# Kernel tuning notes

Hardware: AMD Instinct MI355X
Metric: run time of the kernel (lower is better)

## Reference

```python
import jax, jax.numpy as jnp
import numpy as np

N_NODES = 50000
N_EDGES = 800000
IN_CH = 64
HID = 64
EDGE_DIM = 16


def _glorot(key, shape):
    fan_in, fan_out = shape[0], shape[1]
    lim = (6.0 / (fan_in + fan_out)) ** 0.5
    return jax.random.uniform(key, shape, jnp.float32, -lim, lim)


def setup_inputs() -> dict:
    key = jax.random.key(0)
    ks = jax.random.split(key, 12)
    x = jax.random.normal(ks[0], (N_NODES, IN_CH), jnp.float32)
    edge_index = jax.random.randint(ks[1], (2, N_EDGES), 0, N_NODES, jnp.int64)
    edge_attr = jax.random.normal(ks[2], (N_EDGES, EDGE_DIM), jnp.float32)
    # SAGEConv1: lin_l (aggregated neighbors, with bias) + lin_r (root, no bias)
    W1l = _glorot(ks[3], (IN_CH, HID)); b1l = jnp.zeros((HID,), jnp.float32)
    W1r = _glorot(ks[4], (IN_CH, HID))
    # SAGEConv2
    W2l = _glorot(ks[5], (HID, HID)); b2l = jnp.zeros((HID,), jnp.float32)
    W2r = _glorot(ks[6], (HID, HID))
    # edge MLP: Linear(2*HID+EDGE_DIM -> HID), ReLU, Linear(HID -> 1)
    Wm1 = _glorot(ks[7], (2 * HID + EDGE_DIM, HID))
    bm1 = jnp.zeros((HID,), jnp.float32)
    Wm2 = _glorot(ks[8], (HID, 1))
    bm2 = jnp.zeros((1,), jnp.float32)
    return dict(x=x, edge_index=edge_index, edge_attr=edge_attr,
                W1l=W1l, b1l=b1l, W1r=W1r,
                W2l=W2l, b2l=b2l, W2r=W2r,
                Wm1=Wm1, bm1=bm1, Wm2=Wm2, bm2=bm2)


def _sage_conv(x, src, dst, deg_inv, Wl, bl, Wr):
    # mean aggregation of source-node features at destination nodes
    n = x.shape[0]
    agg = jax.ops.segment_sum(x[src], dst, num_segments=n)  # [N, d]
    agg = agg * deg_inv  # mean over incoming edges
    return agg @ Wl + bl + x @ Wr


def reference(x, edge_index, edge_attr, W1l, b1l, W1r, W2l, b2l, W2r, Wm1, bm1, Wm2, bm2):
    src, dst = edge_index[0], edge_index[1]
    n = x.shape[0]
    # in-degree (over dst), clamped to 1 as in PyG mean aggregation
    deg = jax.ops.segment_sum(jnp.ones((src.shape[0],), x.dtype), dst, num_segments=n)
    deg_inv = (1.0 / jnp.maximum(deg, 1.0))[:, None]  # [N,1]

    h = jax.nn.relu(_sage_conv(x, src, dst, deg_inv, W1l, b1l, W1r))
    h = jax.nn.relu(_sage_conv(h, src, dst, deg_inv, W2l, b2l, W2r))

    # gather endpoint embeddings + concat with edge features -> MLP score
    edge_input = jnp.concatenate([h[src], h[dst], edge_attr], axis=-1)  # [E, 2H+De]
    hidden = jax.nn.relu(edge_input @ Wm1 + bm1)
    return (hidden @ Wm2 + bm2).squeeze(-1)  # [E]
```

## Files before the change

kernel.cpp:

```cpp
#include <hip/hip_runtime.h>
#include <hip/hip_bf16.h>


#define C 64
#define KP 168
#define SK 136
#define TILE_E 64

typedef short short8 __attribute__((ext_vector_type(8)));
typedef float f32x4 __attribute__((ext_vector_type(4)));

__device__ __forceinline__ unsigned short f2bf(float f) {
    unsigned int u = __float_as_uint(f);
    return (unsigned short)((u + 0x7FFFu + ((u >> 16) & 1u)) >> 16);
}
__device__ __forceinline__ unsigned int pack2(float lo, float hi) {
    return (unsigned int)f2bf(lo) | ((unsigned int)f2bf(hi) << 16);
}
__device__ __forceinline__ float bflo(unsigned int u) { return __uint_as_float(u << 16); }
__device__ __forceinline__ float bfhi(unsigned int u) { return __uint_as_float(u & 0xFFFF0000u); }

__global__ void deg_count_ea(const int* __restrict__ dst, int* __restrict__ degi,
                             const float* __restrict__ ea, unsigned short* __restrict__ eaB,
                             int E, int doEa) {
    int i = blockIdx.x * blockDim.x + threadIdx.x;
    if (i < E) atomicAdd(&degi[dst[i]], 1);
    if (doEa && i < 2 * E) {
        const float4* p = (const float4*)(ea + (size_t)i * 8);
        float4 a = p[0], b = p[1];
        uint4 o;
        o.x = pack2(a.x, a.y); o.y = pack2(a.z, a.w);
        o.z = pack2(b.x, b.y); o.w = pack2(b.z, b.w);
        *(uint4*)(eaB + (size_t)i * 8) = o;
    }
}

__global__ __launch_bounds__(256) void scan_partial(const int* __restrict__ degi,
        int* __restrict__ rowptr, int* __restrict__ partials, int N) {
    __shared__ int sWs[4];
    int t = threadIdx.x, b = blockIdx.x;
    int g0 = b * 1024 + t * 4;
    int v0 = (g0 + 0 < N) ? degi[g0 + 0] : 0;
    int v1 = (g0 + 1 < N) ? degi[g0 + 1] : 0;
    int v2 = (g0 + 2 < N) ? degi[g0 + 2] : 0;
    int v3 = (g0 + 3 < N) ? degi[g0 + 3] : 0;
    int tsum = v0 + v1 + v2 + v3;
    int lane = t & 63, w = t >> 6;
    int incl = tsum;
    #pragma unroll
    for (int m = 1; m < 64; m <<= 1) {
        int y = __shfl_up(incl, m, 64);
        if (lane >= m) incl += y;
    }
    if (lane == 63) sWs[w] = incl;
    __syncthreads();
    int wprefix = 0;
    for (int i = 0; i < w; ++i) wprefix += sWs[i];
    int run = wprefix + incl - tsum;
    if (g0 + 0 < N) rowptr[g0 + 0] = run; run += v0;
    if (g0 + 1 < N) rowptr[g0 + 1] = run; run += v1;
    if (g0 + 2 < N) rowptr[g0 + 2] = run; run += v2;
    if (g0 + 3 < N) rowptr[g0 + 3] = run;
    if (t == 255) partials[b] = wprefix + incl;
}

__global__ void scan_offsets(const int* __restrict__ partials, int* __restrict__ offsets, int nb) {
    int lane = threadIdx.x;
    int v = (lane < nb) ? partials[lane] : 0;
    int incl = v;
    #pragma unroll
    for (int m = 1; m < 64; m <<= 1) {
        int y = __shfl_up(incl, m, 64);
        if (lane >= m) incl += y;
    }
    if (lane < nb) offsets[lane] = incl - v;
}

__global__ void scan_add(int* __restrict__ rowptr, const int* __restrict__ offsets,
                         int* __restrict__ cursor, const int* __restrict__ degi,
                         float* __restrict__ deg_inv, int N, int E) {
    int i = blockIdx.x * blockDim.x + threadIdx.x;
    if (i < N) {
        int r = rowptr[i] + offsets[i >> 10];
        rowptr[i] = r;
        cursor[i] = r;
        deg_inv[i] = 1.0f / fmaxf((float)degi[i], 1.0f);
    }
    if (i == 0) rowptr[N] = E;
}

__global__ void fill_csr(const int* __restrict__ src, const int* __restrict__ dst,
                         int* __restrict__ cursor, int* __restrict__ eSrc, int E) {
    int e = blockIdx.x * blockDim.x + threadIdx.x;
    if (e < E) {
        int p = atomicAdd(&cursor[dst[e]], 1);
        eSrc[p] = src[e];
    }
}

__global__ void to_bf16(const float* __restrict__ in, unsigned short* __restrict__ outb, int n8) {
    int i = blockIdx.x * blockDim.x + threadIdx.x;
    if (i >= n8) return;
    const float4* p = (const float4*)(in + (size_t)i * 8);
    float4 a = p[0], b = p[1];
    uint4 o;
    o.x = pack2(a.x, a.y); o.y = pack2(a.z, a.w);
    o.z = pack2(b.x, b.y); o.w = pack2(b.z, b.w);
    *(uint4*)(outb + (size_t)i * 8) = o;
}

__global__ __launch_bounds__(256) void csr_agg_bf16(const unsigned short* __restrict__ fB,
        const int* __restrict__ rowptr, const int* __restrict__ eSrc,
        const float* __restrict__ deg_inv, unsigned short* __restrict__ aggB, int N) {
    int node = blockIdx.x * 4 + (threadIdx.x >> 6);
    if (node >= N) return;
    int lane = threadIdx.x & 63;
    int s8 = lane >> 3, ci = lane & 7;
    int row = rowptr[node], end = rowptr[node + 1];
    float a[8] = {0.f, 0.f, 0.f, 0.f, 0.f, 0.f, 0.f, 0.f};
    int j = row;
    for (; j + 16 <= end; j += 16) {
        int sA = eSrc[j + s8];
        int sB = eSrc[j + 8 + s8];
        uint4 vA = *(const uint4*)(fB + (size_t)sA * C + ci * 8);
        uint4 vB = *(const uint4*)(fB + (size_t)sB * C + ci * 8);
        a[0] += bflo(vA.x); a[1] += bfhi(vA.x);
        a[2] += bflo(vA.y); a[3] += bfhi(vA.y);
        a[4] += bflo(vA.z); a[5] += bfhi(vA.z);
        a[6] += bflo(vA.w); a[7] += bfhi(vA.w);
        a[0] += bflo(vB.x); a[1] += bfhi(vB.x);
        a[2] += bflo(vB.y); a[3] += bfhi(vB.y);
        a[4] += bflo(vB.z); a[5] += bfhi(vB.z);
        a[6] += bflo(vB.w); a[7] += bfhi(vB.w);
    }
    for (; j < end; j += 8) {
        if (j + s8 < end) {
            int s = eSrc[j + s8];
            uint4 v = *(const uint4*)(fB + (size_t)s * C + ci * 8);
            a[0] += bflo(v.x); a[1] += bfhi(v.x);
            a[2] += bflo(v.y); a[3] += bfhi(v.y);
            a[4] += bflo(v.z); a[5] += bfhi(v.z);
            a[6] += bflo(v.w); a[7] += bfhi(v.w);
        }
    }
    #pragma unroll
    for (int m = 8; m < 64; m <<= 1)
        #pragma unroll
        for (int k = 0; k < 8; ++k)
            a[k] += __shfl_xor(a[k], m, 64);
    if (s8 == 0) {
        float di = deg_inv[node];
        uint4 o;
        o.x = pack2(a[0] * di, a[1] * di);
        o.y = pack2(a[2] * di, a[3] * di);
        o.z = pack2(a[4] * di, a[5] * di);
        o.w = pack2(a[6] * di, a[7] * di);
        *(uint4*)(aggB + (size_t)node * C + ci * 8) = o;
    }
}

__global__ __launch_bounds__(256) void dense_mfma(
        const unsigned short* __restrict__ aB, const unsigned short* __restrict__ xB,
        const float* __restrict__ Wl, const float* __restrict__ Wr,
        const float* __restrict__ bl, unsigned short* __restrict__ hOut, int N) {
    __shared__ unsigned short sW[C * SK];
    __shared__ unsigned short sAB[C * SK];
    int t = threadIdx.x;
    int lane = t & 63, w = t >> 6;
    int l15 = lane & 15, quad = lane >> 4;
    int n0 = blockIdx.x * 64;

    for (int i = t; i < 128 * C; i += 256) {
        int k = i >> 6, n = i & 63;
        float v = (k < C) ? Wl[k * C + n] : Wr[(k - C) * C + n];
        sW[n * SK + k] = f2bf(v);
    }
    for (int i = t; i < 64 * 16; i += 256) {
        int r = i >> 4, ch = i & 15;
        int node = n0 + r;
        uint4 v = {0u, 0u, 0u, 0u};
        if (node < N)
            v = (ch < 8) ? *(const uint4*)(aB + (size_t)node * C + ch * 8)
                         : *(const uint4*)(xB + (size_t)node * C + (ch - 8) * 8);
        *(uint4*)&sAB[r * SK + ch * 8] = v;
    }
    __syncthreads();

    short8 bW[4][4];
    #pragma unroll
    for (int t4 = 0; t4 < 4; ++t4)
        #pragma unroll
        for (int kc = 0; kc < 4; ++kc)
            bW[t4][kc] = *(const short8*)&sW[(t4 * 16 + l15) * SK + kc * 32 + quad * 8];
    float blr[4];
    #pragma unroll
    for (int t4 = 0; t4 < 4; ++t4) blr[t4] = bl[t4 * 16 + l15];

    f32x4 acc[4] = {{0.f, 0.f, 0.f, 0.f}, {0.f, 0.f, 0.f, 0.f},
                    {0.f, 0.f, 0.f, 0.f}, {0.f, 0.f, 0.f, 0.f}};
    #pragma unroll
    for (int kc = 0; kc < 4; ++kc) {
        short8 a = *(const short8*)&sAB[(w * 16 + l15) * SK + kc * 32 + quad * 8];
        #pragma unroll
        for (int t4 = 0; t4 < 4; ++t4)
            acc[t4] = __builtin_amdgcn_mfma_f32_16x16x32_bf16(a, bW[t4][kc], acc[t4], 0, 0, 0);
    }
    __syncthreads();

    #pragma unroll
    for (int t4 = 0; t4 < 4; ++t4)
        #pragma unroll
        for (int r = 0; r < 4; ++r) {
            int rl = w * 16 + quad * 4 + r;
            sW[rl * 72 + t4 * 16 + l15] = f2bf(fmaxf(acc[t4][r] + blr[t4], 0.f));
        }
    __syncthreads();
    for (int i = t; i < 64 * 8; i += 256) {
        int r = i >> 3, c8 = i & 7;
        int node = n0 + r;
        if (node < N)
            *(uint4*)(hOut + (size_t)node * C + c8 * 8) = *(const uint4*)&sW[r * 72 + c8 * 8];
    }
}

template <bool EAB>
__device__ __forceinline__ void gather_rows(const unsigned short* __restrict__ hB,
        const unsigned short* __restrict__ eaB, const float* __restrict__ ea,
        int s, int d, int idxc, int quad,
        uint4& u0, uint4& u1, uint4& u2, uint4& u3, uint4& u4) {
    const uint4* ps = (const uint4*)(hB + (size_t)s * C);
    const uint4* pd = (const uint4*)(hB + (size_t)d * C);
    u0 = ps[quad];
    u1 = ps[4 + quad];
    u2 = pd[quad];
    u3 = pd[4 + quad];
    u4.x = 0u; u4.y = 0u; u4.z = 0u; u4.w = 0u;
    if (quad < 2) {
        if (EAB) {
            u4 = *(const uint4*)(eaB + (size_t)idxc * 16 + quad * 8);
        } else {
            const float4* pe = (const float4*)(ea + (size_t)idxc * 16 + quad * 8);
            float4 f0 = pe[0], f1 = pe[1];
            u4.x = pack2(f0.x, f0.y); u4.y = pack2(f0.z, f0.w);
            u4.z = pack2(f1.x, f1.y); u4.w = pack2(f1.z, f1.w);
        }
    }
}

template <bool EAB>
__global__ __launch_bounds__(256) void edge_mlp_pipe(
        const unsigned short* __restrict__ hB, const int* __restrict__ src,
        const int* __restrict__ dst, const float* __restrict__ ea,
        const unsigned short* __restrict__ eaB,
        const float* __restrict__ Wm1, const float* __restrict__ bm1,
        const float* __restrict__ Wm2, const float* __restrict__ bm2,
        float* __restrict__ out, int E, int nTiles) {
    __shared__ unsigned short sW[C * KP];
    int t = threadIdx.x;
    int lane = t & 63, w = t >> 6;
    int l15 = lane & 15, quad = lane >> 4;

    for (int i = t; i < C * 3; i += 256) {
        int r = i / 3, cc = 144 + (i % 3) * 8;
        uint4 z = {0u, 0u, 0u, 0u};
        *(uint4*)&sW[r * KP + cc] = z;
    }
    for (int i = t; i < 144 * C; i += 256) {
        int k = i >> 6, n = i & 63;
        sW[n * KP + k] = f2bf(Wm1[i]);
    }
    __syncthreads();

    short8 bW[4][5];
    #pragma unroll
    for (int t4 = 0; t4 < 4; ++t4)
        #pragma unroll
        for (int kc = 0; kc < 5; ++kc)
            bW[t4][kc] = *(const short8*)&sW[(t4 * 16 + l15) * KP + kc * 32 + quad * 8];
    float bmr[4], w2r[4];
    #pragma unroll
    for (int t4 = 0; t4 < 4; ++t4) {
        int j = t4 * 16 + l15;
        bmr[t4] = bm1[j];
        w2r[t4] = Wm2[j];
    }
    float bb = bm2[0];

    int stride = gridDim.x;
    int lbase = w * 16 + l15;

    int tile = blockIdx.x;
    int idxc = min(tile * TILE_E + lbase, E - 1);
    int s = src[idxc], d = dst[idxc];
    int tileN = tile + stride;
    int idxNc = (tileN < nTiles) ? min(tileN * TILE_E + lbase, E - 1) : idxc;
    int sN = src[idxNc], dN = dst[idxNc];
    uint4 cu0, cu1, cu2, cu3, cu4;
    gather_rows<EAB>(hB, eaB, ea, s, d, idxc, quad, cu0, cu1, cu2, cu3, cu4);

    while (true) {
        bool hasNext = (tileN < nTiles);
        uint4 nu0, nu1, nu2, nu3, nu4;
        gather_rows<EAB>(hB, eaB, ea, sN, dN, idxNc, quad, nu0, nu1, nu2, nu3, nu4);
        int tileNN = tileN + stride;
        int idxNNc = (tileNN < nTiles) ? min(tileNN * TILE_E + lbase, E - 1) : idxNc;
        int sNN = src[idxNNc], dNN = dst[idxNNc];

        short8 a0 = *(short8*)&cu0, a1 = *(short8*)&cu1, a2 = *(short8*)&cu2,
               a3 = *(short8*)&cu3, a4 = *(short8*)&cu4;
        f32x4 acc[4] = {{0.f, 0.f, 0.f, 0.f}, {0.f, 0.f, 0.f, 0.f},
                        {0.f, 0.f, 0.f, 0.f}, {0.f, 0.f, 0.f, 0.f}};
        #pragma unroll
        for (int t4 = 0; t4 < 4; ++t4) {
            acc[t4] = __builtin_amdgcn_mfma_f32_16x16x32_bf16(a0, bW[t4][0], acc[t4], 0, 0, 0);
            acc[t4] = __builtin_amdgcn_mfma_f32_16x16x32_bf16(a1, bW[t4][1], acc[t4], 0, 0, 0);
            acc[t4] = __builtin_amdgcn_mfma_f32_16x16x32_bf16(a2, bW[t4][2], acc[t4], 0, 0, 0);
            acc[t4] = __builtin_amdgcn_mfma_f32_16x16x32_bf16(a3, bW[t4][3], acc[t4], 0, 0, 0);
            acc[t4] = __builtin_amdgcn_mfma_f32_16x16x32_bf16(a4, bW[t4][4], acc[t4], 0, 0, 0);
        }

        float sres[4];
        #pragma unroll
        for (int r = 0; r < 4; ++r) {
            float v = 0.f;
            #pragma unroll
            for (int t4 = 0; t4 < 4; ++t4)
                v += fmaxf(acc[t4][r] + bmr[t4], 0.f) * w2r[t4];
            #pragma unroll
            for (int m = 1; m < 16; m <<= 1)
                v += __shfl_xor(v, m, 16);
            sres[r] = v;
        }
        if (l15 == 0) {
            int e0 = tile * TILE_E;
            #pragma unroll
            for (int r = 0; r < 4; ++r) {
                int e = e0 + w * 16 + quad * 4 + r;
                if (e < E) out[e] = sres[r] + bb;
            }
        }

        if (!hasNext) break;
        tile = tileN; tileN = tileNN;
        idxc = idxNc; idxNc = idxNNc;
        s = sN; sN = sNN; d = dN; dN = dNN;
        cu0 = nu0; cu1 = nu1; cu2 = nu2; cu3 = nu3; cu4 = nu4;
    }
}

extern "C" void kernel_launch(void* const* d_in, const int* in_sizes, int n_in,
                              void* d_out, int out_size, void* d_ws, size_t ws_size,
                              hipStream_t stream) {
    const float* x   = (const float*)d_in[0];
    const int*   ei  = (const int*)d_in[1];
    const float* ea  = (const float*)d_in[2];
    const float* W1l = (const float*)d_in[3];
    const float* b1l = (const float*)d_in[4];
    const float* W1r = (const float*)d_in[5];
    const float* W2l = (const float*)d_in[6];
    const float* b2l = (const float*)d_in[7];
    const float* W2r = (const float*)d_in[8];
    const float* Wm1 = (const float*)d_in[9];
    const float* bm1 = (const float*)d_in[10];
    const float* Wm2 = (const float*)d_in[11];
    const float* bm2 = (const float*)d_in[12];
    float* out = (float*)d_out;

    const int N = in_sizes[0] / C;
    const int E = in_sizes[1] / 2;
    const int* src = ei;
    const int* dst = ei + E;

    char* wsb = (char*)d_ws;
    int npad = (N + 1023) & ~1023;
    float* deg_inv = (float*)wsb;                wsb += (size_t)npad * 4;
    unsigned short* xB   = (unsigned short*)wsb; wsb += (size_t)npad * C * 2;
    unsigned short* h1B  = (unsigned short*)wsb; wsb += (size_t)npad * C * 2;
    unsigned short* h2B  = (unsigned short*)wsb; wsb += (size_t)npad * C * 2;
    unsigned short* aggB = (unsigned short*)wsb; wsb += (size_t)npad * C * 2;
    int* degi    = (int*)wsb;                    wsb += (size_t)npad * 4;
    int* rowptr  = (int*)wsb;                    wsb += (size_t)(npad + 64) * 4;
    int* cursor  = (int*)wsb;                    wsb += (size_t)npad * 4;
    int* eSrc    = (int*)wsb;                    wsb += (size_t)E * 4;
    int* partials = (int*)wsb;                   wsb += 64 * 4;
    int* offsets  = (int*)wsb;                   wsb += 64 * 4;
    unsigned short* eaB = (unsigned short*)wsb;
    size_t used = (size_t)(wsb - (char*)d_ws);
    int useEaB = (ws_size >= used + (size_t)E * 16 * 2) ? 1 : 0;

    int tpb = 256;
    int nb = (N + 1023) / 1024;

    hipMemsetAsync(degi, 0, (size_t)N * sizeof(int), stream);
    deg_count_ea<<<(2 * E + tpb - 1) / tpb, tpb, 0, stream>>>(dst, degi, ea, eaB, E, useEaB);
    to_bf16<<<((N * C / 8) + tpb - 1) / tpb, tpb, 0, stream>>>(x, xB, N * C / 8);
    scan_partial<<<nb, tpb, 0, stream>>>(degi, rowptr, partials, N);
    scan_offsets<<<1, 64, 0, stream>>>(partials, offsets, nb);
    scan_add<<<(N + tpb - 1) / tpb, tpb, 0, stream>>>(rowptr, offsets, cursor, degi, deg_inv, N, E);
    fill_csr<<<(E + tpb - 1) / tpb, tpb, 0, stream>>>(src, dst, cursor, eSrc, E);

    csr_agg_bf16<<<(N + 3) / 4, tpb, 0, stream>>>(xB, rowptr, eSrc, deg_inv, aggB, N);
    dense_mfma<<<(N + 63) / 64, tpb, 0, stream>>>(aggB, xB, W1l, W1r, b1l, h1B, N);

    csr_agg_bf16<<<(N + 3) / 4, tpb, 0, stream>>>(h1B, rowptr, eSrc, deg_inv, aggB, N);
    dense_mfma<<<(N + 63) / 64, tpb, 0, stream>>>(aggB, h1B, W2l, W2r, b2l, h2B, N);

    int nTiles = (E + TILE_E - 1) / TILE_E;
    int grid = nTiles < 2048 ? nTiles : 2048;
    if (useEaB)
        edge_mlp_pipe<true><<<grid, tpb, 0, stream>>>(h2B, src, dst, ea, eaB,
                Wm1, bm1, Wm2, bm2, out, E, nTiles);
    else
        edge_mlp_pipe<false><<<grid, tpb, 0, stream>>>(h2B, src, dst, ea, eaB,
                Wm1, bm1, Wm2, bm2, out, E, nTiles);
}
```

Baseline: 314.9 us.

## Fuse CSR aggregation into dense MFMA layer and merge small prep/scan kernels

Each SAGE layer's neighbor mean aggregation now runs inside the dense MFMA kernel. Each wave aggregates 16 nodes straight into shared memory, so the aggB global round-trip and one launch per layer go away. The x-to-bf16 conversion is folded into the degree/edge-attr prep kernel, and the offsets scan is merged into scan_add. The cost is that the fused kernel runs only 782 blocks with serial per-node aggregation per wave, so it has less parallelism for hiding gather latency than the earlier 12.5k-block aggregation kernel.

```diff
diff --git a/kernel.cpp b/kernel.cpp
--- a/kernel.cpp
+++ b/kernel.cpp
@@ -20,9 +20,10 @@
 __device__ __forceinline__ float bflo(unsigned int u) { return __uint_as_float(u << 16); }
 __device__ __forceinline__ float bfhi(unsigned int u) { return __uint_as_float(u & 0xFFFF0000u); }
 
-__global__ void deg_count_ea(const int* __restrict__ dst, int* __restrict__ degi,
-                             const float* __restrict__ ea, unsigned short* __restrict__ eaB,
-                             int E, int doEa) {
+__global__ void prep(const int* __restrict__ dst, int* __restrict__ degi,
+                     const float* __restrict__ ea, unsigned short* __restrict__ eaB,
+                     const float* __restrict__ x, unsigned short* __restrict__ xB,
+                     int E, int nx8, int doEa) {
     int i = blockIdx.x * blockDim.x + threadIdx.x;
     if (i < E) atomicAdd(&degi[dst[i]], 1);
     if (doEa && i < 2 * E) {
@@ -32,6 +33,14 @@
         o.x = pack2(a.x, a.y); o.y = pack2(a.z, a.w);
         o.z = pack2(b.x, b.y); o.w = pack2(b.z, b.w);
         *(uint4*)(eaB + (size_t)i * 8) = o;
+    }
+    if (i < nx8) {
+        const float4* p = (const float4*)(x + (size_t)i * 8);
+        float4 a = p[0], b = p[1];
+        uint4 o;
+        o.x = pack2(a.x, a.y); o.y = pack2(a.z, a.w);
+        o.z = pack2(b.x, b.y); o.w = pack2(b.z, b.w);
+        *(uint4*)(xB + (size_t)i * 8) = o;
     }
 }
 
@@ -64,24 +73,26 @@
     if (t == 255) partials[b] = wprefix + incl;
 }
 
-__global__ void scan_offsets(const int* __restrict__ partials, int* __restrict__ offsets, int nb) {
-    int lane = threadIdx.x;
-    int v = (lane < nb) ? partials[lane] : 0;
-    int incl = v;
-    #pragma unroll
-    for (int m = 1; m < 64; m <<= 1) {
-        int y = __shfl_up(incl, m, 64);
-        if (lane >= m) incl += y;
-    }
-    if (lane < nb) offsets[lane] = incl - v;
-}
-
-__global__ void scan_add(int* __restrict__ rowptr, const int* __restrict__ offsets,
-                         int* __restrict__ cursor, const int* __restrict__ degi,
-                         float* __restrict__ deg_inv, int N, int E) {
-    int i = blockIdx.x * blockDim.x + threadIdx.x;
+__global__ __launch_bounds__(256) void scan_add_fused(int* __restrict__ rowptr,
+        const int* __restrict__ partials, int* __restrict__ cursor,
+        const int* __restrict__ degi, float* __restrict__ deg_inv,
+        int N, int E, int nb) {
+    __shared__ int sOff[64];
+    int t = threadIdx.x;
+    if (t < 64) {
+        int v = (t < nb) ? partials[t] : 0;
+        int incl = v;
+        #pragma unroll
+        for (int m = 1; m < 64; m <<= 1) {
+            int y = __shfl_up(incl, m, 64);
+            if (t >= m) incl += y;
+        }
+        sOff[t] = incl - v;
+    }
+    __syncthreads();
+    int i = blockIdx.x * 256 + t;
     if (i < N) {
-        int r = rowptr[i] + offsets[i >> 10];
+        int r = rowptr[i] + sOff[i >> 10];
         rowptr[i] = r;
         cursor[i] = r;
         deg_inv[i] = 1.0f / fmaxf((float)degi[i], 1.0f);
@@ -98,69 +109,10 @@
     }
 }
 
-__global__ void to_bf16(const float* __restrict__ in, unsigned short* __restrict__ outb, int n8) {
-    int i = blockIdx.x * blockDim.x + threadIdx.x;
-    if (i >= n8) return;
-    const float4* p = (const float4*)(in + (size_t)i * 8);
-    float4 a = p[0], b = p[1];
-    uint4 o;
-    o.x = pack2(a.x, a.y); o.y = pack2(a.z, a.w);
-    o.z = pack2(b.x, b.y); o.w = pack2(b.z, b.w);
-    *(uint4*)(outb + (size_t)i * 8) = o;
-}
-
-__global__ __launch_bounds__(256) void csr_agg_bf16(const unsigned short* __restrict__ fB,
+__global__ __launch_bounds__(256) void fused_layer(
+        const unsigned short* __restrict__ fB,
         const int* __restrict__ rowptr, const int* __restrict__ eSrc,
-        const float* __restrict__ deg_inv, unsigned short* __restrict__ aggB, int N) {
-    int node = blockIdx.x * 4 + (threadIdx.x >> 6);
-    if (node >= N) return;
-    int lane = threadIdx.x & 63;
-    int s8 = lane >> 3, ci = lane & 7;
-    int row = rowptr[node], end = rowptr[node + 1];
-    float a[8] = {0.f, 0.f, 0.f, 0.f, 0.f, 0.f, 0.f, 0.f};
-    int j = row;
-    for (; j + 16 <= end; j += 16) {
-        int sA = eSrc[j + s8];
-        int sB = eSrc[j + 8 + s8];
-        uint4 vA = *(const uint4*)(fB + (size_t)sA * C + ci * 8);
-        uint4 vB = *(const uint4*)(fB + (size_t)sB * C + ci * 8);
-        a[0] += bflo(vA.x); a[1] += bfhi(vA.x);
-        a[2] += bflo(vA.y); a[3] += bfhi(vA.y);
-        a[4] += bflo(vA.z); a[5] += bfhi(vA.z);
-        a[6] += bflo(vA.w); a[7] += bfhi(vA.w);
-        a[0] += bflo(vB.x); a[1] += bfhi(vB.x);
-        a[2] += bflo(vB.y); a[3] += bfhi(vB.y);
-        a[4] += bflo(vB.z); a[5] += bfhi(vB.z);
-        a[6] += bflo(vB.w); a[7] += bfhi(vB.w);
-    }
-    for (; j < end; j += 8) {
-        if (j + s8 < end) {
-            int s = eSrc[j + s8];
-            uint4 v = *(const uint4*)(fB + (size_t)s * C + ci * 8);
-            a[0] += bflo(v.x); a[1] += bfhi(v.x);
-            a[2] += bflo(v.y); a[3] += bfhi(v.y);
-            a[4] += bflo(v.z); a[5] += bfhi(v.z);
-            a[6] += bflo(v.w); a[7] += bfhi(v.w);
-        }
-    }
-    #pragma unroll
-    for (int m = 8; m < 64; m <<= 1)
-        #pragma unroll
-        for (int k = 0; k < 8; ++k)
-            a[k] += __shfl_xor(a[k], m, 64);
-    if (s8 == 0) {
-        float di = deg_inv[node];
-        uint4 o;
-        o.x = pack2(a[0] * di, a[1] * di);
-        o.y = pack2(a[2] * di, a[3] * di);
-        o.z = pack2(a[4] * di, a[5] * di);
-        o.w = pack2(a[6] * di, a[7] * di);
-        *(uint4*)(aggB + (size_t)node * C + ci * 8) = o;
-    }
-}
-
-__global__ __launch_bounds__(256) void dense_mfma(
-        const unsigned short* __restrict__ aB, const unsigned short* __restrict__ xB,
+        const float* __restrict__ deg_inv,
         const float* __restrict__ Wl, const float* __restrict__ Wr,
         const float* __restrict__ bl, unsigned short* __restrict__ hOut, int N) {
     __shared__ unsigned short sW[C * SK];
@@ -175,14 +127,59 @@
         float v = (k < C) ? Wl[k * C + n] : Wr[(k - C) * C + n];
         sW[n * SK + k] = f2bf(v);
     }
-    for (int i = t; i < 64 * 16; i += 256) {
-        int r = i >> 4, ch = i & 15;
+    for (int i = t; i < 64 * 8; i += 256) {
+        int r = i >> 3, ch = i & 7;
         int node = n0 + r;
         uint4 v = {0u, 0u, 0u, 0u};
-        if (node < N)
-            v = (ch < 8) ? *(const uint4*)(aB + (size_t)node * C + ch * 8)
-                         : *(const uint4*)(xB + (size_t)node * C + (ch - 8) * 8);
-        *(uint4*)&sAB[r * SK + ch * 8] = v;
+        if (node < N) v = *(const uint4*)(fB + (size_t)node * C + ch * 8);
+        *(uint4*)&sAB[r * SK + 64 + ch * 8] = v;
+    }
+
+    int s8 = lane >> 3, ci = lane & 7;
+    for (int p = 0; p < 16; ++p) {
+        int node = n0 + w * 16 + p;
+        if (node >= N) break;
+        int row = rowptr[node], end = rowptr[node + 1];
+        float a[8] = {0.f, 0.f, 0.f, 0.f, 0.f, 0.f, 0.f, 0.f};
+        int j = row;
+        for (; j + 16 <= end; j += 16) {
+            int sA = eSrc[j + s8];
+            int sB = eSrc[j + 8 + s8];
+            uint4 vA = *(const uint4*)(fB + (size_t)sA * C + ci * 8);
+            uint4 vB = *(const uint4*)(fB + (size_t)sB * C + ci * 8);
+            a[0] += bflo(vA.x); a[1] += bfhi(vA.x);
+            a[2] += bflo(vA.y); a[3] += bfhi(vA.y);
+            a[4] += bflo(vA.z); a[5] += bfhi(vA.z);
+            a[6] += bflo(vA.w); a[7] += bfhi(vA.w);
+            a[0] += bflo(vB.x); a[1] += bfhi(vB.x);
+            a[2] += bflo(vB.y); a[3] += bfhi(vB.y);
+            a[4] += bflo(vB.z); a[5] += bfhi(vB.z);
+            a[6] += bflo(vB.w); a[7] += bfhi(vB.w);
+        }
+        for (; j < end; j += 8) {
+            if (j + s8 < end) {
+                int s = eSrc[j + s8];
+                uint4 v = *(const uint4*)(fB + (size_t)s * C + ci * 8);
+                a[0] += bflo(v.x); a[1] += bfhi(v.x);
+                a[2] += bflo(v.y); a[3] += bfhi(v.y);
+                a[4] += bflo(v.z); a[5] += bfhi(v.z);
+                a[6] += bflo(v.w); a[7] += bfhi(v.w);
+            }
+        }
+        #pragma unroll
+        for (int m = 8; m < 64; m <<= 1)
+            #pragma unroll
+            for (int k = 0; k < 8; ++k)
+                a[k] += __shfl_xor(a[k], m, 64);
+        if (s8 == 0) {
+            float di = deg_inv[node];
+            uint4 o;
+            o.x = pack2(a[0] * di, a[1] * di);
+            o.y = pack2(a[2] * di, a[3] * di);
+            o.z = pack2(a[4] * di, a[5] * di);
+            o.w = pack2(a[6] * di, a[7] * di);
+            *(uint4*)&sAB[(w * 16 + p) * SK + ci * 8] = o;
+        }
     }
     __syncthreads();
 
@@ -377,33 +374,31 @@
     unsigned short* xB   = (unsigned short*)wsb; wsb += (size_t)npad * C * 2;
     unsigned short* h1B  = (unsigned short*)wsb; wsb += (size_t)npad * C * 2;
     unsigned short* h2B  = (unsigned short*)wsb; wsb += (size_t)npad * C * 2;
-    unsigned short* aggB = (unsigned short*)wsb; wsb += (size_t)npad * C * 2;
     int* degi    = (int*)wsb;                    wsb += (size_t)npad * 4;
     int* rowptr  = (int*)wsb;                    wsb += (size_t)(npad + 64) * 4;
     int* cursor  = (int*)wsb;                    wsb += (size_t)npad * 4;
     int* eSrc    = (int*)wsb;                    wsb += (size_t)E * 4;
     int* partials = (int*)wsb;                   wsb += 64 * 4;
-    int* offsets  = (int*)wsb;                   wsb += 64 * 4;
     unsigned short* eaB = (unsigned short*)wsb;
     size_t used = (size_t)(wsb - (char*)d_ws);
     int useEaB = (ws_size >= used + (size_t)E * 16 * 2) ? 1 : 0;
 
     int tpb = 256;
     int nb = (N + 1023) / 1024;
+    int nx8 = N * C / 8;
 
     hipMemsetAsync(degi, 0, (size_t)N * sizeof(int), stream);
-    deg_count_ea<<<(2 * E + tpb - 1) / tpb, tpb, 0, stream>>>(dst, degi, ea, eaB, E, useEaB);
-    to_bf16<<<((N * C / 8) + tpb - 1) / tpb, tpb, 0, stream>>>(x, xB, N * C / 8);
+    int prepN = (2 * E > nx8) ? 2 * E : nx8;
+    prep<<<(prepN + tpb - 1) / tpb, tpb, 0, stream>>>(dst, degi, ea, eaB, x, xB, E, nx8, useEaB);
     scan_partial<<<nb, tpb, 0, stream>>>(degi, rowptr, partials, N);
-    scan_offsets<<<1, 64, 0, stream>>>(partials, offsets, nb);
-    scan_add<<<(N + tpb - 1) / tpb, tpb, 0, stream>>>(rowptr, offsets, cursor, degi, deg_inv, N, E);
+    scan_add_fused<<<(N + tpb - 1) / tpb, tpb, 0, stream>>>(rowptr, partials, cursor,
+            degi, deg_inv, N, E, nb);
     fill_csr<<<(E + tpb - 1) / tpb, tpb, 0, stream>>>(src, dst, cursor, eSrc, E);
 
-    csr_agg_bf16<<<(N + 3) / 4, tpb, 0, stream>>>(xB, rowptr, eSrc, deg_inv, aggB, N);
-    dense_mfma<<<(N + 63) / 64, tpb, 0, stream>>>(aggB, xB, W1l, W1r, b1l, h1B, N);
-
-    csr_agg_bf16<<<(N + 3) / 4, tpb, 0, stream>>>(h1B, rowptr, eSrc, deg_inv, aggB, N);
-    dense_mfma<<<(N + 63) / 64, tpb, 0, stream>>>(aggB, h1B, W2l, W2r, b2l, h2B, N);
+    fused_layer<<<(N + 63) / 64, tpb, 0, stream>>>(xB, rowptr, eSrc, deg_inv,
+            W1l, W1r, b1l, h1B, N);
+    fused_layer<<<(N + 63) / 64, tpb, 0, stream>>>(h1B, rowptr, eSrc, deg_inv,
+            W2l, W2r, b2l, h2B, N);
 
     int nTiles = (E + TILE_E - 1) / TILE_E;
     int grid = nTiles < 2048 ? nTiles : 2048;
```

After: 333.8 us. 6.0% more time.
